# Kernel optimization log

Measured on AMD Instinct MI355X. Metric: run time of the kernel, lower is better.

## Reference

```python
import jax, jax.numpy as jnp
import numpy as np

D_MODEL = 1024
N_HEADS = 16
D_HEAD = D_MODEL // N_HEADS  # 64
SCALE = 1.0 / float(np.sqrt(D_HEAD))


def setup_inputs() -> dict:
    key = jax.random.key(0)
    kx, kq, kk, kv, ko = jax.random.split(key, 5)
    B, L = 1, 4096
    x = jax.random.normal(kx, (B, L, D_MODEL), dtype=jnp.float32)
    init = 0.02  # small init so softmax isn't saturated
    Wq = jax.random.normal(kq, (D_MODEL, D_MODEL), dtype=jnp.float32) * init
    Wk = jax.random.normal(kk, (D_MODEL, D_MODEL), dtype=jnp.float32) * init
    Wv = jax.random.normal(kv, (D_MODEL, D_MODEL), dtype=jnp.float32) * init
    Wo = jax.random.normal(ko, (D_MODEL, D_MODEL), dtype=jnp.float32) * init
    return {"x": x, "Wq": Wq, "Wk": Wk, "Wv": Wv, "Wo": Wo}


def reference(x, Wq, Wk, Wv, Wo):
    # x: [B, L, d_model]; torch Linear (no bias): y = x @ W.T
    B, L, _ = x.shape

    def split_heads(t):  # [B, L, d_model] -> [B, H, L, Dh]
        return t.reshape(B, L, N_HEADS, D_HEAD).transpose(0, 2, 1, 3)

    q = split_heads(x @ Wq.T)
    k = split_heads(x @ Wk.T)
    v = split_heads(x @ Wv.T)

    # Full (non-flash) attention: explicit [B, H, L, L] scores (causal=False, eval dropout=0)
    scores = jnp.einsum("bhld,bhmd->bhlm", q, k) * SCALE
    attn = jax.nn.softmax(scores, axis=-1)
    out = jnp.einsum("bhlm,bhmd->bhld", attn, v)

    out = out.transpose(0, 2, 1, 3).reshape(B, L, D_MODEL)
    return out @ Wo.T
```

## Files before the change

### kernel.cpp

```cpp
#include <hip/hip_runtime.h>

typedef _Float16 f16_t;
typedef _Float16 f16x4 __attribute__((ext_vector_type(4)));
typedef _Float16 f16x8 __attribute__((ext_vector_type(8)));
typedef float f32x4 __attribute__((ext_vector_type(4)));

#define D_MODEL 1024
#define LSEQ 4096
#define NH 16
#define DH 64
#define QSCALE 0.18033688011112042f

#define GLDS16(g, l)                                                     \
    __builtin_amdgcn_global_load_lds(                                    \
        (const __attribute__((address_space(1))) void*)(g),              \
        (__attribute__((address_space(3))) void*)(l), 16, 0, 0)

#define WAIT_VM(n) asm volatile("s_waitcnt vmcnt(" #n ")" ::: "memory")

__global__ __launch_bounds__(256) void cvt_x(const float* __restrict__ in,
                                             f16_t* __restrict__ out, int n) {
    int i = (blockIdx.x * 256 + threadIdx.x) * 4;
    if (i + 3 < n) {
        float4 v = *(const float4*)&in[i];
        alignas(8) f16_t o4[4] = {(f16_t)v.x, (f16_t)v.y, (f16_t)v.z, (f16_t)v.w};
        *(uint2*)&out[i] = *(const uint2*)o4;
    }
}

__global__ __launch_bounds__(256) void cvt_w4(const float* __restrict__ w0,
                                              const float* __restrict__ w1,
                                              const float* __restrict__ w2,
                                              const float* __restrict__ w3,
                                              f16_t* __restrict__ out) {
    const int q = blockIdx.y;
    const float* src = (q == 0) ? w0 : (q == 1) ? w1 : (q == 2) ? w2 : w3;
    const float scale = (q == 0) ? QSCALE : 1.f;
    int i = (blockIdx.x * 256 + threadIdx.x) * 4;
    float4 v = *(const float4*)&src[i];
    alignas(8) f16_t o4[4] = {(f16_t)(v.x * scale), (f16_t)(v.y * scale),
                              (f16_t)(v.z * scale), (f16_t)(v.w * scale)};
    *(uint2*)&out[(size_t)q * (D_MODEL * D_MODEL) + i] = *(const uint2*)o4;
}

__global__ __launch_bounds__(256, 3) void gemm_f16(const f16_t* __restrict__ A,
                                                   const f16_t* __restrict__ B,
                                                   void* __restrict__ Cout,
                                                   int M, int N, int K, int mode) {
    __shared__ alignas(16) f16_t As[3][128 * 32];
    __shared__ alignas(16) f16_t Bs[3][128 * 32];

    const int tid  = threadIdx.x;
    const int wave = tid >> 6;
    const int lane = tid & 63;
    const int quad = lane >> 4;
    const int l16  = lane & 15;
    const int wm = (wave & 1) * 64;
    const int wn = (wave >> 1) * 64;
    const int bm = blockIdx.x * 128;
    const int bn = blockIdx.y * 128;

    f32x4 acc[4][4] = {};
    const int nk = K / 32;

    auto stage = [&](int kt, int b) {
        const int c0 = wave * 2;
        GLDS16(&A[(size_t)(bm + c0 * 16 + l16) * K + kt * 32 + quad * 8],
               &As[b][c0 * 512]);
        GLDS16(&A[(size_t)(bm + (c0 + 1) * 16 + l16) * K + kt * 32 + quad * 8],
               &As[b][(c0 + 1) * 512]);
        GLDS16(&B[(size_t)(bn + c0 * 16 + l16) * K + kt * 32 + quad * 8],
               &Bs[b][c0 * 512]);
        GLDS16(&B[(size_t)(bn + (c0 + 1) * 16 + l16) * K + kt * 32 + quad * 8],
               &Bs[b][(c0 + 1) * 512]);
    };

    stage(0, 0);
    stage(1, 1);
    for (int kt = 0; kt < nk; ++kt) {
        const int cb = kt % 3;
        if (kt < nk - 1) WAIT_VM(4);
        else             WAIT_VM(0);
        __syncthreads();
        if (kt + 2 < nk) stage(kt + 2, (kt + 2) % 3);

        f16x8 af[4], bfr[4];
#pragma unroll
        for (int mt = 0; mt < 4; ++mt)
            af[mt] = *(const f16x8*)&As[cb][((wm >> 4) + mt) * 512 + lane * 8];
#pragma unroll
        for (int nt = 0; nt < 4; ++nt)
            bfr[nt] = *(const f16x8*)&Bs[cb][((wn >> 4) + nt) * 512 + lane * 8];
#pragma unroll
        for (int mt = 0; mt < 4; ++mt)
#pragma unroll
            for (int nt = 0; nt < 4; ++nt)
                acc[mt][nt] = __builtin_amdgcn_mfma_f32_16x16x32_f16(
                    bfr[nt], af[mt], acc[mt][nt], 0, 0, 0);
    }

#pragma unroll
    for (int mt = 0; mt < 4; ++mt)
#pragma unroll
        for (int nt = 0; nt < 4; ++nt) {
            int row = bm + wm + mt * 16 + l16;
            int col = bn + wn + nt * 16 + quad * 4;
            if (mode == 0) {
                f16x4 p = {(f16_t)acc[mt][nt][0], (f16_t)acc[mt][nt][1],
                           (f16_t)acc[mt][nt][2], (f16_t)acc[mt][nt][3]};
                *(f16x4*)&((f16_t*)Cout)[((size_t)(col >> 6) * M + row) * 64 +
                                         (col & 63)] = p;
            } else {
                *(f32x4*)&((float*)Cout)[(size_t)row * N + col] = acc[mt][nt];
            }
        }
}

__global__ __launch_bounds__(256) void transpose_v(const f16_t* __restrict__ vh,
                                                   f16_t* __restrict__ vt) {
    __shared__ f16_t Ts[64][72];
    const int t = threadIdx.x;
    const int lt = blockIdx.x;
    const int head = blockIdx.y;

#pragma unroll
    for (int i = 0; i < 2; ++i) {
        int idx = t + i * 256;
        int row = idx >> 3, part = idx & 7;
        *(uint4*)&Ts[row][part * 8] =
            *(const uint4*)&vh[((size_t)head * LSEQ + lt * 64 + row) * DH + part * 8];
    }
    __syncthreads();
#pragma unroll
    for (int i = 0; i < 2; ++i) {
        int idx = t + i * 256;
        int d = idx >> 3, part = idx & 7;
        alignas(16) f16_t p8[8];
#pragma unroll
        for (int j = 0; j < 8; ++j) p8[j] = Ts[part * 8 + j][d];
        *(uint4*)&vt[((size_t)head * DH + d) * LSEQ + lt * 64 + part * 8] =
            *(const uint4*)p8;
    }
}

__global__ __launch_bounds__(512, 2) void attn_kernel(const f16_t* __restrict__ qh,
                                                      const f16_t* __restrict__ kh,
                                                      const f16_t* __restrict__ vt,
                                                      f16_t* __restrict__ ao) {
    __shared__ alignas(16) f16_t Ks[2][2][8 * 512];
    __shared__ alignas(16) f16_t Vs[2][2][8 * 512];
    __shared__ alignas(16) f16_t Ps[8 * 4096];

    const int tid  = threadIdx.x;
    const int wave = tid >> 6;
    const int lane = tid & 63;
    const int quad = lane >> 4;
    const int l16  = lane & 15;
    const int wq   = wave & 3;
    const int kha  = wave >> 2;

    const int id = blockIdx.x;
    const int head = id & 15;
    const int qrow0 = (id >> 4) * 256 + wq * 64;
    const int key0 = kha * (LSEQ / 2);

    const f16_t* Q  = qh + (size_t)head * LSEQ * DH;
    const f16_t* K  = kh + (size_t)head * LSEQ * DH;
    const f16_t* Vt = vt + (size_t)head * DH * LSEQ;

    f16x8 qf[4][2];
#pragma unroll
    for (int qt = 0; qt < 4; ++qt)
#pragma unroll
        for (int kc = 0; kc < 2; ++kc)
            qf[qt][kc] = *(const f16x8*)
                &Q[(size_t)(qrow0 + qt * 16 + l16) * DH + kc * 32 + quad * 8];

    f32x4 o[4][4] = {};
    float lp[4] = {0.f, 0.f, 0.f, 0.f};

    auto stage = [&](int kt, int b) {
        const int j0 = wq * 2;
#pragma unroll
        for (int jj = 0; jj < 2; ++jj) {
            const int j = j0 + jj, mt = j >> 1, kc = j & 1;
            GLDS16(&K[(size_t)(key0 + kt * 64 + mt * 16 + l16) * DH + kc * 32 +
                      quad * 8],
                   &Ks[kha][b][j * 512]);
            GLDS16(&Vt[(size_t)(mt * 16 + l16) * LSEQ + key0 + kt * 64 + kc * 32 +
                       quad * 8],
                   &Vs[kha][b][j * 512]);
        }
    };

    const int NT = LSEQ / 2 / 64;
    stage(0, 0);
    for (int kt = 0; kt < NT; ++kt) {
        const int cb = kt & 1;
        WAIT_VM(0);
        __syncthreads();
        if (kt + 1 < NT) stage(kt + 1, cb ^ 1);

        f16x8 kf[4][2], vf[4][2];
#pragma unroll
        for (int mt = 0; mt < 4; ++mt)
#pragma unroll
            for (int kc = 0; kc < 2; ++kc)
                kf[mt][kc] = *(const f16x8*)&Ks[kha][cb][(mt * 2 + kc) * 512 +
                                                         lane * 8];
#pragma unroll
        for (int dt = 0; dt < 4; ++dt)
#pragma unroll
            for (int kc = 0; kc < 2; ++kc)
                vf[dt][kc] = *(const f16x8*)&Vs[kha][cb][(dt * 2 + kc) * 512 +
                                                         lane * 8];

        f32x4 s[4][4] = {};
#pragma unroll
        for (int mt = 0; mt < 4; ++mt)
#pragma unroll
            for (int qt = 0; qt < 4; ++qt)
#pragma unroll
                for (int kc = 0; kc < 2; ++kc)
                    s[mt][qt] = __builtin_amdgcn_mfma_f32_16x16x32_f16(
                        kf[mt][kc], qf[qt][kc], s[mt][qt], 0, 0, 0);

#pragma unroll
        for (int mt = 0; mt < 4; ++mt)
#pragma unroll
            for (int qt = 0; qt < 4; ++qt) {
                float e0 = __builtin_amdgcn_exp2f(s[mt][qt][0]);
                float e1 = __builtin_amdgcn_exp2f(s[mt][qt][1]);
                float e2 = __builtin_amdgcn_exp2f(s[mt][qt][2]);
                float e3 = __builtin_amdgcn_exp2f(s[mt][qt][3]);
                lp[qt] += (e0 + e1) + (e2 + e3);
                f16x4 p = {(f16_t)e0, (f16_t)e1, (f16_t)e2, (f16_t)e3};
                int qr = qt * 16 + l16;
                int key2 = (mt * 16 + quad * 4) ^ ((qr & 7) << 3);
                *(f16x4*)&Ps[wave * 4096 + qr * 64 + key2] = p;
            }
        __builtin_amdgcn_wave_barrier();

        f16x8 pf[4][2];
#pragma unroll
        for (int qt = 0; qt < 4; ++qt)
#pragma unroll
            for (int kc = 0; kc < 2; ++kc) {
                int qr = qt * 16 + l16;
                int keys = (kc * 32 + quad * 8) ^ ((qr & 7) << 3);
                pf[qt][kc] = *(const f16x8*)&Ps[wave * 4096 + qr * 64 + keys];
            }

#pragma unroll
        for (int dt = 0; dt < 4; ++dt)
#pragma unroll
            for (int qt = 0; qt < 4; ++qt)
#pragma unroll
                for (int kc = 0; kc < 2; ++kc)
                    o[dt][qt] = __builtin_amdgcn_mfma_f32_16x16x32_f16(
                        vf[dt][kc], pf[qt][kc], o[dt][qt], 0, 0, 0);
        __builtin_amdgcn_wave_barrier();
    }

    __syncthreads();
    float* scr  = (float*)Ps;
    float* lscr = (float*)Vs;
    if (wave >= 4) {
#pragma unroll
        for (int dt = 0; dt < 4; ++dt)
#pragma unroll
            for (int qt = 0; qt < 4; ++qt)
                *(f32x4*)&scr[(((wave - 4) * 16 + dt * 4 + qt) * 64 + lane) * 4] =
                    o[dt][qt];
#pragma unroll
        for (int qt = 0; qt < 4; ++qt)
            lscr[((wave - 4) * 4 + qt) * 64 + lane] = lp[qt];
    }
    __syncthreads();
    if (wave < 4) {
#pragma unroll
        for (int dt = 0; dt < 4; ++dt)
#pragma unroll
            for (int qt = 0; qt < 4; ++qt)
                o[dt][qt] += *(const f32x4*)
                    &scr[((wave * 16 + dt * 4 + qt) * 64 + lane) * 4];
#pragma unroll
        for (int qt = 0; qt < 4; ++qt) {
            float t = lp[qt] + lscr[(wave * 4 + qt) * 64 + lane];
            t += __shfl_xor(t, 16, 64);
            t += __shfl_xor(t, 32, 64);
            lp[qt] = 1.f / t;
        }
#pragma unroll
        for (int dt = 0; dt < 4; ++dt)
#pragma unroll
            for (int qt = 0; qt < 4; ++qt) {
                f16x4 ov = {(f16_t)(o[dt][qt][0] * lp[qt]),
                            (f16_t)(o[dt][qt][1] * lp[qt]),
                            (f16_t)(o[dt][qt][2] * lp[qt]),
                            (f16_t)(o[dt][qt][3] * lp[qt])};
                int qrow = qrow0 + qt * 16 + l16;
                *(f16x4*)&ao[(size_t)qrow * D_MODEL + head * 64 + dt * 16 +
                             quad * 4] = ov;
            }
    }
}

extern "C" void kernel_launch(void* const* d_in, const int* in_sizes, int n_in,
                              void* d_out, int out_size, void* d_ws, size_t ws_size,
                              hipStream_t stream) {
    const float* x  = (const float*)d_in[0];
    const float* Wq = (const float*)d_in[1];
    const float* Wk = (const float*)d_in[2];
    const float* Wv = (const float*)d_in[3];
    const float* Wo = (const float*)d_in[4];

    f16_t* xb = (f16_t*)d_ws;
    f16_t* wq = xb + (size_t)LSEQ * D_MODEL;
    f16_t* wo = wq + (size_t)3 * D_MODEL * D_MODEL;
    f16_t* qh = wo + (size_t)D_MODEL * D_MODEL;
    f16_t* kh = qh + (size_t)LSEQ * D_MODEL;
    f16_t* vh = kh + (size_t)LSEQ * D_MODEL;
    f16_t* vt = vh + (size_t)LSEQ * D_MODEL;
    f16_t* ao = vt + (size_t)LSEQ * D_MODEL;

    const int nx = LSEQ * D_MODEL;
    cvt_x<<<nx / 1024, 256, 0, stream>>>(x, xb, nx);
    cvt_w4<<<dim3(D_MODEL * D_MODEL / 1024, 4), 256, 0, stream>>>(Wq, Wk, Wv, Wo, wq);

    gemm_f16<<<dim3(LSEQ / 128, 3 * D_MODEL / 128), 256, 0, stream>>>(
        xb, wq, qh, LSEQ, 3 * D_MODEL, D_MODEL, 0);

    transpose_v<<<dim3(LSEQ / 64, NH), 256, 0, stream>>>(vh, vt);

    attn_kernel<<<dim3((LSEQ / 256) * NH), 512, 0, stream>>>(qh, kh, vt, ao);

    gemm_f16<<<dim3(LSEQ / 128, D_MODEL / 128), 256, 0, stream>>>(
        ao, wo, d_out, LSEQ, D_MODEL, D_MODEL, 1);
}
```

Baseline: 259.7 us.

## Keep softmax probabilities in registers and feed PV MFMA directly

The attention kernel no longer writes exponentiated scores to LDS and reads them back. It now uses the S accumulator layout directly as the B operand of 16x16x16 MFMAs for the PV product, processing one key subtile at a time. To support this, V is pre-permuted by the transpose kernel into a 16x4 fragment layout matching the MFMA operand. The P LDS buffer is removed, which reduces shared memory and may raise occupancy. In exchange the PV step uses the smaller-K MFMA (16x16x16 instead of 16x16x32) and converts with round-toward-zero packing.

```diff
diff --git a/kernel.cpp b/kernel.cpp
--- a/kernel.cpp
+++ b/kernel.cpp
@@ -1,6 +1,8 @@
 #include <hip/hip_runtime.h>
 
 typedef _Float16 f16_t;
+typedef __fp16 fp16x2 __attribute__((ext_vector_type(2)));
+typedef _Float16 f16x2 __attribute__((ext_vector_type(2)));
 typedef _Float16 f16x4 __attribute__((ext_vector_type(4)));
 typedef _Float16 f16x8 __attribute__((ext_vector_type(8)));
 typedef float f32x4 __attribute__((ext_vector_type(4)));
@@ -117,7 +119,7 @@
 }
 
 __global__ __launch_bounds__(256) void transpose_v(const f16_t* __restrict__ vh,
-                                                   f16_t* __restrict__ vt) {
+                                                   f16_t* __restrict__ v4) {
     __shared__ f16_t Ts[64][72];
     const int t = threadIdx.x;
     const int lt = blockIdx.x;
@@ -131,25 +133,30 @@
             *(const uint4*)&vh[((size_t)head * LSEQ + lt * 64 + row) * DH + part * 8];
     }
     __syncthreads();
-#pragma unroll
-    for (int i = 0; i < 2; ++i) {
-        int idx = t + i * 256;
-        int d = idx >> 3, part = idx & 7;
-        alignas(16) f16_t p8[8];
-#pragma unroll
-        for (int j = 0; j < 8; ++j) p8[j] = Ts[part * 8 + j][d];
-        *(uint4*)&vt[((size_t)head * DH + d) * LSEQ + lt * 64 + part * 8] =
-            *(const uint4*)p8;
-    }
+
+    const int c   = t >> 4;
+    const int dt  = c >> 2, kb = c & 3;
+    const int km2 = (t & 15) >> 2;
+    const int dl2 = t & 3;
+    alignas(16) f16_t buf[16];
+#pragma unroll
+    for (int i = 0; i < 16; ++i) {
+        int j = i & 3, dd = i >> 2;
+        buf[i] = Ts[kb * 16 + km2 * 4 + j][dt * 16 + dl2 * 4 + dd];
+    }
+    f16_t* dst = v4 + (size_t)head * (LSEQ * DH) + lt * 4096 + c * 256 + (t & 15) * 16;
+    *(uint4*)&dst[0] = *(const uint4*)&buf[0];
+    *(uint4*)&dst[8] = *(const uint4*)&buf[8];
 }
 
 __global__ __launch_bounds__(512, 2) void attn_kernel(const f16_t* __restrict__ qh,
                                                       const f16_t* __restrict__ kh,
-                                                      const f16_t* __restrict__ vt,
+                                                      const f16_t* __restrict__ v4,
                                                       f16_t* __restrict__ ao) {
-    __shared__ alignas(16) f16_t Ks[2][2][8 * 512];
-    __shared__ alignas(16) f16_t Vs[2][2][8 * 512];
-    __shared__ alignas(16) f16_t Ps[8 * 4096];
+    __shared__ alignas(16) f16_t smem[32768];
+    __shared__ alignas(16) float lscr[16 * 64];
+    f16_t* KsB = smem;
+    f16_t* VsB = smem + 16384;
 
     const int tid  = threadIdx.x;
     const int wave = tid >> 6;
@@ -162,11 +169,10 @@
     const int id = blockIdx.x;
     const int head = id & 15;
     const int qrow0 = (id >> 4) * 256 + wq * 64;
-    const int key0 = kha * (LSEQ / 2);
 
     const f16_t* Q  = qh + (size_t)head * LSEQ * DH;
     const f16_t* K  = kh + (size_t)head * LSEQ * DH;
-    const f16_t* Vt = vt + (size_t)head * DH * LSEQ;
+    const f16_t* V4 = v4 + (size_t)head * (LSEQ * DH);
 
     f16x8 qf[4][2];
 #pragma unroll
@@ -180,16 +186,16 @@
     float lp[4] = {0.f, 0.f, 0.f, 0.f};
 
     auto stage = [&](int kt, int b) {
-        const int j0 = wq * 2;
+        f16_t* ks = KsB + (kha * 2 + b) * 4096;
+        f16_t* vs = VsB + (kha * 2 + b) * 4096;
+        const int ktg = kha * 32 + kt;
 #pragma unroll
         for (int jj = 0; jj < 2; ++jj) {
-            const int j = j0 + jj, mt = j >> 1, kc = j & 1;
-            GLDS16(&K[(size_t)(key0 + kt * 64 + mt * 16 + l16) * DH + kc * 32 +
-                      quad * 8],
-                   &Ks[kha][b][j * 512]);
-            GLDS16(&Vt[(size_t)(mt * 16 + l16) * LSEQ + key0 + kt * 64 + kc * 32 +
-                       quad * 8],
-                   &Vs[kha][b][j * 512]);
+            const int j = wq * 2 + jj;
+            GLDS16(&K[(size_t)(ktg * 64 + wq * 16 + l16) * DH + jj * 32 + quad * 8],
+                   &ks[j * 512]);
+            GLDS16(&V4[(size_t)ktg * 4096 + wq * 1024 + jj * 512 + lane * 8],
+                   &vs[wq * 1024 + jj * 512]);
         }
     };
 
@@ -201,70 +207,51 @@
         __syncthreads();
         if (kt + 1 < NT) stage(kt + 1, cb ^ 1);
 
-        f16x8 kf[4][2], vf[4][2];
-#pragma unroll
-        for (int mt = 0; mt < 4; ++mt)
-#pragma unroll
-            for (int kc = 0; kc < 2; ++kc)
-                kf[mt][kc] = *(const f16x8*)&Ks[kha][cb][(mt * 2 + kc) * 512 +
-                                                         lane * 8];
-#pragma unroll
-        for (int dt = 0; dt < 4; ++dt)
-#pragma unroll
-            for (int kc = 0; kc < 2; ++kc)
-                vf[dt][kc] = *(const f16x8*)&Vs[kha][cb][(dt * 2 + kc) * 512 +
-                                                         lane * 8];
-
-        f32x4 s[4][4] = {};
-#pragma unroll
-        for (int mt = 0; mt < 4; ++mt)
-#pragma unroll
-            for (int qt = 0; qt < 4; ++qt)
-#pragma unroll
-                for (int kc = 0; kc < 2; ++kc)
-                    s[mt][qt] = __builtin_amdgcn_mfma_f32_16x16x32_f16(
-                        kf[mt][kc], qf[qt][kc], s[mt][qt], 0, 0, 0);
-
-#pragma unroll
-        for (int mt = 0; mt < 4; ++mt)
+        const f16_t* ks = KsB + (kha * 2 + cb) * 4096;
+        const f16_t* vs = VsB + (kha * 2 + cb) * 4096;
+
+#pragma unroll
+        for (int mt = 0; mt < 4; ++mt) {
+            f16x8 kf0 = *(const f16x8*)&ks[(mt * 2 + 0) * 512 + lane * 8];
+            f16x8 kf1 = *(const f16x8*)&ks[(mt * 2 + 1) * 512 + lane * 8];
+
+            f32x4 s[4] = {};
 #pragma unroll
             for (int qt = 0; qt < 4; ++qt) {
-                float e0 = __builtin_amdgcn_exp2f(s[mt][qt][0]);
-                float e1 = __builtin_amdgcn_exp2f(s[mt][qt][1]);
-                float e2 = __builtin_amdgcn_exp2f(s[mt][qt][2]);
-                float e3 = __builtin_amdgcn_exp2f(s[mt][qt][3]);
+                s[qt] = __builtin_amdgcn_mfma_f32_16x16x32_f16(kf0, qf[qt][0],
+                                                               s[qt], 0, 0, 0);
+                s[qt] = __builtin_amdgcn_mfma_f32_16x16x32_f16(kf1, qf[qt][1],
+                                                               s[qt], 0, 0, 0);
+            }
+
+            f16x4 vfd[4];
+#pragma unroll
+            for (int dt = 0; dt < 4; ++dt)
+                vfd[dt] = *(const f16x4*)&vs[(dt * 4 + mt) * 256 + lane * 4];
+
+#pragma unroll
+            for (int qt = 0; qt < 4; ++qt) {
+                float e0 = __builtin_amdgcn_exp2f(s[qt][0]);
+                float e1 = __builtin_amdgcn_exp2f(s[qt][1]);
+                float e2 = __builtin_amdgcn_exp2f(s[qt][2]);
+                float e3 = __builtin_amdgcn_exp2f(s[qt][3]);
                 lp[qt] += (e0 + e1) + (e2 + e3);
-                f16x4 p = {(f16_t)e0, (f16_t)e1, (f16_t)e2, (f16_t)e3};
-                int qr = qt * 16 + l16;
-                int key2 = (mt * 16 + quad * 4) ^ ((qr & 7) << 3);
-                *(f16x4*)&Ps[wave * 4096 + qr * 64 + key2] = p;
+                fp16x2 p01 = __builtin_amdgcn_cvt_pkrtz(e0, e1);
+                fp16x2 p23 = __builtin_amdgcn_cvt_pkrtz(e2, e3);
+                f16x4 p = {__builtin_bit_cast(f16x2, p01)[0],
+                           __builtin_bit_cast(f16x2, p01)[1],
+                           __builtin_bit_cast(f16x2, p23)[0],
+                           __builtin_bit_cast(f16x2, p23)[1]};
+#pragma unroll
+                for (int dt = 0; dt < 4; ++dt)
+                    o[dt][qt] = __builtin_amdgcn_mfma_f32_16x16x16f16(
+                        vfd[dt], p, o[dt][qt], 0, 0, 0);
             }
-        __builtin_amdgcn_wave_barrier();
-
-        f16x8 pf[4][2];
-#pragma unroll
-        for (int qt = 0; qt < 4; ++qt)
-#pragma unroll
-            for (int kc = 0; kc < 2; ++kc) {
-                int qr = qt * 16 + l16;
-                int keys = (kc * 32 + quad * 8) ^ ((qr & 7) << 3);
-                pf[qt][kc] = *(const f16x8*)&Ps[wave * 4096 + qr * 64 + keys];
-            }
-
-#pragma unroll
-        for (int dt = 0; dt < 4; ++dt)
-#pragma unroll
-            for (int qt = 0; qt < 4; ++qt)
-#pragma unroll
-                for (int kc = 0; kc < 2; ++kc)
-                    o[dt][qt] = __builtin_amdgcn_mfma_f32_16x16x32_f16(
-                        vf[dt][kc], pf[qt][kc], o[dt][qt], 0, 0, 0);
-        __builtin_amdgcn_wave_barrier();
+        }
     }
 
     __syncthreads();
-    float* scr  = (float*)Ps;
-    float* lscr = (float*)Vs;
+    float* scr = (float*)smem;
     if (wave >= 4) {
 #pragma unroll
         for (int dt = 0; dt < 4; ++dt)
@@ -321,8 +308,8 @@
     f16_t* qh = wo + (size_t)D_MODEL * D_MODEL;
     f16_t* kh = qh + (size_t)LSEQ * D_MODEL;
     f16_t* vh = kh + (size_t)LSEQ * D_MODEL;
-    f16_t* vt = vh + (size_t)LSEQ * D_MODEL;
-    f16_t* ao = vt + (size_t)LSEQ * D_MODEL;
+    f16_t* v4 = vh + (size_t)LSEQ * D_MODEL;
+    f16_t* ao = v4 + (size_t)LSEQ * D_MODEL;
 
     const int nx = LSEQ * D_MODEL;
     cvt_x<<<nx / 1024, 256, 0, stream>>>(x, xb, nx);
@@ -331,9 +318,9 @@
     gemm_f16<<<dim3(LSEQ / 128, 3 * D_MODEL / 128), 256, 0, stream>>>(
         xb, wq, qh, LSEQ, 3 * D_MODEL, D_MODEL, 0);
 
-    transpose_v<<<dim3(LSEQ / 64, NH), 256, 0, stream>>>(vh, vt);
-
-    attn_kernel<<<dim3((LSEQ / 256) * NH), 512, 0, stream>>>(qh, kh, vt, ao);
+    transpose_v<<<dim3(LSEQ / 64, NH), 256, 0, stream>>>(vh, v4);
+
+    attn_kernel<<<dim3((LSEQ / 256) * NH), 512, 0, stream>>>(qh, kh, v4, ao);
 
     gemm_f16<<<dim3(LSEQ / 128, D_MODEL / 128), 256, 0, stream>>>(
         ao, wo, d_out, LSEQ, D_MODEL, D_MODEL, 1);
```

Result: no change. 259.1 us (-0.2%).
